# Performance work log

Hardware: AMD Instinct MI355X
Metric: run time of the kernel (lower is better)

## Reference

```python
import jax, jax.numpy as jnp
import numpy as np
from jax import lax


def log_g(x):
    # log of g(x) = x + 0.5 for x >= 0, sigmoid(x) for x < 0
    return jnp.where(x >= 0, jnp.log(jax.nn.relu(x) + 0.5), -jax.nn.softplus(-x))


def setup_inputs() -> dict:
    key = jax.random.key(0)
    k1, k2, k3, k4 = jax.random.split(key, 4)
    N, L, H_in, H = 8, 4096, 1024, 1024
    x = jax.random.normal(k1, (N, L, H_in), dtype=jnp.float32)
    W = jax.random.normal(k2, (2 * H, H_in), dtype=jnp.float32) * (1.0 / np.sqrt(H_in))
    b = jax.random.normal(k3, (2 * H,), dtype=jnp.float32) * 0.01
    hx = jax.random.uniform(k4, (N, H), dtype=jnp.float32)  # positive initial state
    return {"x": x, "W": W, "b": b, "hx": hx}


def reference(x, W, b, hx):
    # linear_ih: (N, L, 2H)
    zh = jnp.einsum('nli,oi->nlo', x, W) + b
    z, h_inter = jnp.split(zh, 2, axis=-1)  # each (N, L, H)
    log_z = -jax.nn.softplus(-z)            # log sigmoid(z)
    log_coeffs = -jax.nn.softplus(z)        # log (1 - sigmoid(z))
    log_h0 = jnp.log(hx)[:, None, :]        # (N, 1, H)
    log_tilde_h = log_g(h_inter)
    log_values = jnp.concatenate([log_h0, log_z + log_tilde_h], axis=1)  # (N, L+1, H)
    # Heinsen parallel scan in log space
    a_star = jnp.pad(jnp.cumsum(log_coeffs, axis=1), ((0, 0), (1, 0), (0, 0)))  # (N, L+1, H)
    log_h = a_star + lax.cumlogsumexp(log_values - a_star, axis=1)
    h = jnp.exp(log_h)
    return h[:, 1:]  # (N, L, H)
```

## Files before the change

### kernel.cpp

```cpp
#include <hip/hip_runtime.h>
#include <hip/hip_bf16.h>
#include <hip/hip_fp16.h>


#define N_B   8
#define L_SEQ 4096
#define H_DIM 1024
#define K_DIM 1024
#define O_DIM 2048
#define M_TOT (N_B * L_SEQ)

#define BM 128
#define BN 128
#define BK 64

#define NCHUNK 128
#define CLEN   (L_SEQ / NCHUNK)
#define NCH    (N_B * H_DIM)

typedef unsigned short ushort_t;
typedef unsigned short us8 __attribute__((ext_vector_type(8)));
typedef __bf16 v8bf __attribute__((ext_vector_type(8)));
typedef float f32x4 __attribute__((ext_vector_type(4)));

static __device__ __forceinline__ ushort_t f2bf(float f) {
    __hip_bfloat16 h = __float2bfloat16(f);
    return *reinterpret_cast<ushort_t*>(&h);
}

static __device__ __forceinline__ void dma16(const ushort_t* g, ushort_t* l) {
    __builtin_amdgcn_global_load_lds(
        (const __attribute__((address_space(1))) unsigned int*)g,
        (__attribute__((address_space(3))) unsigned int*)l,
        16, 0, 0);
}

__global__ __launch_bounds__(256) void cvt_f32_bf16(
    const float* __restrict__ src, ushort_t* __restrict__ dst)
{
    const int i = blockIdx.x * 256 + threadIdx.x;
    const float4 f0 = ((const float4*)src)[2 * i];
    const float4 f1 = ((const float4*)src)[2 * i + 1];
    us8 o;
    o[0] = f2bf(f0.x); o[1] = f2bf(f0.y); o[2] = f2bf(f0.z); o[3] = f2bf(f0.w);
    o[4] = f2bf(f1.x); o[5] = f2bf(f1.y); o[6] = f2bf(f1.z); o[7] = f2bf(f1.w);
    ((us8*)dst)[i] = o;
}

__global__ __launch_bounds__(256) void cvt_w_perm(
    const float* __restrict__ src, ushort_t* __restrict__ dst,
    const float* __restrict__ b, float* __restrict__ bp)
{
    const int i  = blockIdx.x * 256 + threadIdx.x;
    const int op = i >> 7;
    const int k  = (i & 127) * 8;
    const int B  = op >> 4, t = op & 15;
    const int orig = (B & 1) * 1024 + (B >> 1) * 16 + t;
    const float4* s = (const float4*)(src + (size_t)orig * K_DIM + k);
    const float4 f0 = s[0], f1 = s[1];
    us8 o;
    o[0] = f2bf(f0.x); o[1] = f2bf(f0.y); o[2] = f2bf(f0.z); o[3] = f2bf(f0.w);
    o[4] = f2bf(f1.x); o[5] = f2bf(f1.y); o[6] = f2bf(f1.z); o[7] = f2bf(f1.w);
    *(us8*)(dst + (size_t)op * K_DIM + k) = o;

    if (i < O_DIM) {
        const int Bb = i >> 4, tb = i & 15;
        bp[i] = b[(Bb & 1) * 1024 + (Bb >> 1) * 16 + tb];
    }
}

__device__ __forceinline__ void gate_av(float z, float hi, float& a, float& v)
{
    const float e  = __expf(-z);
    const float sz = 1.0f / (1.0f + e);
    a = e * sz;
    const float g = (hi >= 0.0f) ? (hi + 0.5f)
                                 : (1.0f / (1.0f + __expf(-hi)));
    v = sz * g;
}

__global__ __launch_bounds__(256) void gemm_zh(
    const ushort_t* __restrict__ Xb,
    const ushort_t* __restrict__ Wb,
    const float* __restrict__ biasp,
    __half2* __restrict__ avbuf,
    float* __restrict__ Aar,
    float* __restrict__ Bar,
    int mbase)
{
    __shared__ ushort_t As[BM * BK];
    __shared__ ushort_t Bs[BN * BK];

    const int tid    = threadIdx.x;
    const int wave   = tid >> 6;
    const int lane   = tid & 63;
    const int lane15 = lane & 15;
    const int quad   = lane >> 4;

    const int n0 = blockIdx.x * BN;
    const int m0 = (blockIdx.y + mbase) * BM;

    const int lrow = lane >> 3;
    const int jj   = (lane & 7) ^ lrow;
    const ushort_t* gA = Xb + (size_t)(m0 + wave * 8 + lrow) * K_DIM + jj * 8;
    const ushort_t* gB = Wb + (size_t)(n0 + wave * 8 + lrow) * K_DIM + jj * 8;
    ushort_t* lA = &As[(wave * 8) * BK];
    ushort_t* lB = &Bs[(wave * 8) * BK];

    const int wm = (wave >> 1) * 64;
    const int wn = (wave & 1) * 64;

    int offA[2][4], offB[2][4];
#pragma unroll
    for (int s = 0; s < 2; ++s) {
#pragma unroll
        for (int t = 0; t < 4; ++t) {
            const int rowA = wm + t * 16 + lane15;
            offA[s][t] = rowA * BK + (((s * 4 + quad) ^ (rowA & 7)) * 8);
            const int rowB = wn + t * 16 + lane15;
            offB[s][t] = rowB * BK + (((s * 4 + quad) ^ (rowB & 7)) * 8);
        }
    }

    const f32x4 fzero = {0.f, 0.f, 0.f, 0.f};
    f32x4 acc[4][4];
#pragma unroll
    for (int i = 0; i < 4; ++i)
#pragma unroll
        for (int j = 0; j < 4; ++j)
            acc[i][j] = fzero;

    for (int kt = 0; kt < K_DIM / BK; ++kt) {
        __syncthreads();
#pragma unroll
        for (int r = 0; r < 4; ++r) {
            dma16(gA + (size_t)r * 32 * K_DIM + kt * BK, lA + r * 32 * BK);
            dma16(gB + (size_t)r * 32 * K_DIM + kt * BK, lB + r * 32 * BK);
        }
        __syncthreads();

#pragma unroll
        for (int s = 0; s < 2; ++s) {
            v8bf af[4], bfr[4];
#pragma unroll
            for (int t = 0; t < 4; ++t) af[t]  = *(const v8bf*)(&As[offA[s][t]]);
#pragma unroll
            for (int t = 0; t < 4; ++t) bfr[t] = *(const v8bf*)(&Bs[offB[s][t]]);
#pragma unroll
            for (int i = 0; i < 4; ++i)
#pragma unroll
                for (int j = 0; j < 4; ++j)
                    acc[i][j] = __builtin_amdgcn_mfma_f32_16x16x32_bf16(
                        af[i], bfr[j], acc[i][j], 0, 0, 0);
        }
    }

    float bv[4];
#pragma unroll
    for (int j = 0; j < 4; ++j)
        bv[j] = biasp[n0 + wn + j * 16 + lane15];

    const int chbase = ((n0 + wn) >> 1) + lane15;

    float Ai[4][2], Bi[4][2];

#pragma unroll
    for (int i = 0; i < 4; ++i) {
        float A[2] = {1.f, 1.f};
        float Bc[2] = {0.f, 0.f};
#pragma unroll
        for (int r = 0; r < 4; ++r) {
            const size_t row = (size_t)(m0 + wm + i * 16 + quad * 4 + r);
            __half2* prow = avbuf + row * H_DIM + chbase;
#pragma unroll
            for (int jp = 0; jp < 2; ++jp) {
                const float z  = acc[i][2 * jp][r]     + bv[2 * jp];
                const float hh = acc[i][2 * jp + 1][r] + bv[2 * jp + 1];
                float a, v;
                gate_av(z, hh, a, v);
                const __half2 h2 = __floats2half2_rn(a, v);
                prow[jp * 16] = h2;
                const float2 f = __half22float2(h2);
                Bc[jp] = fmaf(f.x, Bc[jp], f.y);
                A[jp] *= f.x;
            }
        }
#pragma unroll
        for (int jp = 0; jp < 2; ++jp) {
#pragma unroll
            for (int d = 16; d < 64; d <<= 1) {
                const float Ay = __shfl_xor(A[jp],  d);
                const float By = __shfl_xor(Bc[jp], d);
                Bc[jp] = (lane & d) ? fmaf(A[jp], By, Bc[jp])
                                    : fmaf(Ay, Bc[jp], By);
                A[jp] *= Ay;
            }
            Ai[i][jp] = A[jp];
            Bi[i][jp] = Bc[jp];
        }
    }

    if (lane < 16) {
#pragma unroll
        for (int cc = 0; cc < 2; ++cc) {
            const int grow = m0 + wm + cc * 32;
            const int n    = grow >> 12;
            const int cch  = (grow & (L_SEQ - 1)) >> 5;
            const size_t o = (size_t)cch * NCH + (size_t)n * H_DIM + chbase;
#pragma unroll
            for (int jp = 0; jp < 2; ++jp) {
                const float A0 = Ai[2 * cc][jp],     B0 = Bi[2 * cc][jp];
                const float A1 = Ai[2 * cc + 1][jp], B1 = Bi[2 * cc + 1][jp];
                Aar[o + jp * 16] = A1 * A0;
                Bar[o + jp * 16] = fmaf(A1, B0, B1);
            }
        }
    }
}

__global__ __launch_bounds__(256) void scan_phase2(
    const float* __restrict__ Aar, const float* __restrict__ Bar,
    const float* __restrict__ hx, float* __restrict__ seed)
{
    const int ch = blockIdx.x * 256 + threadIdx.x;
    float carry = hx[ch];
#pragma unroll 8
    for (int c = 0; c < NCHUNK; ++c) {
        seed[c * NCH + ch] = carry;
        carry = fmaf(Aar[c * NCH + ch], carry, Bar[c * NCH + ch]);
    }
}

__global__ __launch_bounds__(256) void scan_phase3(
    const __half2* __restrict__ avbuf,
    const float* __restrict__ seed, float* __restrict__ out)
{
    const int idx = blockIdx.x * 256 + threadIdx.x;
    const int h4  = (idx & 255) << 2;
    const int n   = (idx >> 8) & 7;
    const int c   = idx >> 11;
    const size_t base = ((size_t)(n * L_SEQ + c * CLEN)) * H_DIM + h4;
    const float4* avp = (const float4*)(avbuf + base);
    float* op = out + base;

    const size_t so = (size_t)c * NCH + n * H_DIM + h4;
    float h0[4];
    *(f32x4*)h0 = *(const f32x4*)(seed + so);

#pragma unroll 8
    for (int s = 0; s < CLEN; ++s) {
        float4 avr = avp[(size_t)s * (H_DIM / 4)];
        const __half2* a2 = (const __half2*)&avr;
#pragma unroll
        for (int j = 0; j < 4; ++j) {
            const float2 av = __half22float2(a2[j]);
            h0[j] = fmaf(av.x, h0[j], av.y);
        }
        f32x4 hv = *(const f32x4*)h0;
        __builtin_nontemporal_store(hv, (f32x4*)(op + (size_t)s * H_DIM));
    }
}

extern "C" void kernel_launch(void* const* d_in, const int* in_sizes, int n_in,
                              void* d_out, int out_size, void* d_ws, size_t ws_size,
                              hipStream_t stream)
{
    const float* X    = (const float*)d_in[0];
    const float* Wm   = (const float*)d_in[1];
    const float* bias = (const float*)d_in[2];
    const float* hx   = (const float*)d_in[3];
    float* out = (float*)d_out;

    char* ws = (char*)d_ws;
    ushort_t* wb   = (ushort_t*)ws;
    __half2*  avbuf = (__half2*)(ws + (size_t)O_DIM * K_DIM * 2);
    float*    seed = (float*)((char*)avbuf + (size_t)M_TOT * H_DIM * 4);
    float*    biasp = seed + (size_t)NCHUNK * NCH;

    ushort_t* xb = (ushort_t*)d_out;
    float* Aar = out + (size_t)M_TOT * H_DIM / 2;
    float* Bar = Aar + (size_t)NCHUNK * NCH;

    cvt_w_perm<<<O_DIM * K_DIM / 8 / 256, 256, 0, stream>>>(Wm, wb, bias, biasp);
    cvt_f32_bf16<<<M_TOT * K_DIM / 8 / 256, 256, 0, stream>>>(X, xb);

    dim3 ggrid(O_DIM / BN, (M_TOT / BM) / 4);
    for (int q = 0; q < 4; ++q)
        gemm_zh<<<ggrid, 256, 0, stream>>>(xb, wb, biasp, avbuf, Aar, Bar,
                                           q * 64);

    scan_phase2<<<NCH / 256, 256, 0, stream>>>(Aar, Bar, hx, seed);

    const int p3_blocks = (NCH / 4) * NCHUNK / 256;
    scan_phase3<<<p3_blocks, 256, 0, stream>>>(avbuf, seed, out);
}
```

Before: 478.1 us.

## Double-buffer GEMM with 256-wide tiles, 8 waves, and interleaved DMA/MFMA schedule

```diff
diff --git a/kernel.cpp b/kernel.cpp
--- a/kernel.cpp
+++ b/kernel.cpp
@@ -11,8 +11,9 @@
 #define M_TOT (N_B * L_SEQ)
 
 #define BM 128
-#define BN 128
+#define BN 256
 #define BK 64
+#define KTILES (K_DIM / BK)
 
 #define NCHUNK 128
 #define CLEN   (L_SEQ / NCHUNK)
@@ -79,48 +80,100 @@
     v = sz * g;
 }
 
-__global__ __launch_bounds__(256) void gemm_zh(
+
+#define STG_A(b, kt, r) dma16(gA + (size_t)(r) * 64 * K_DIM + (size_t)(kt) * BK, \
+                              &As[b][((r) * 64 + wave * 8) * BK])
+#define STG_B(b, kt, r) dma16(gB + (size_t)(r) * 64 * K_DIM + (size_t)(kt) * BK, \
+                              &Bs[b][((r) * 64 + wave * 8) * BK])
+
+#define RD_HALF(NA, NB, rb, h)                                                \
+    _Pragma("unroll") for (int i2_ = 0; i2_ < 2; ++i2_)                       \
+    _Pragma("unroll") for (int s_ = 0; s_ < 2; ++s_) {                        \
+        NA[(h) * 2 + i2_][s_] = *(const v8bf*)&As[rb][offA[(h) * 2 + i2_][s_]]; \
+        NB[(h) * 2 + i2_][s_] = *(const v8bf*)&Bs[rb][offB[(h) * 2 + i2_][s_]]; \
+    }
+
+#define QUAD(p, CA, CB) {                                                     \
+    const int ih_ = (p) >> 1, jh_ = (p) & 1;                                  \
+    _Pragma("unroll") for (int i2_ = 0; i2_ < 2; ++i2_)                       \
+    _Pragma("unroll") for (int j2_ = 0; j2_ < 2; ++j2_)                       \
+    _Pragma("unroll") for (int s_ = 0; s_ < 2; ++s_)                          \
+        acc[ih_ * 2 + i2_][jh_ * 2 + j2_] =                                   \
+            __builtin_amdgcn_mfma_f32_16x16x32_bf16(                          \
+                CA[ih_ * 2 + i2_][s_], CB[jh_ * 2 + j2_][s_],                 \
+                acc[ih_ * 2 + i2_][jh_ * 2 + j2_], 0, 0, 0); }
+
+#define BAR() __builtin_amdgcn_s_barrier()
+#define PRIO(x) __builtin_amdgcn_s_setprio(x)
+
+#define TILE(t, cb, CA, CB, NA, NB, sg, rd)                                   \
+    {                                                                         \
+                                                                      \
+        if (sg) { STG_A(cb, (t) + 2, 0); STG_A(cb, (t) + 2, 1); }             \
+        BAR();                                                                \
+        PRIO(1); QUAD(0, CA, CB); PRIO(0);                                    \
+        BAR();                                                                \
+                                                                      \
+        if (sg) { STG_B(cb, (t) + 2, 0); STG_B(cb, (t) + 2, 1); }             \
+        BAR();                                                                \
+        PRIO(1); QUAD(1, CA, CB); PRIO(0);                                    \
+        BAR();                                                                \
+                                                                      \
+        if (sg) { STG_B(cb, (t) + 2, 2); }                                    \
+        if (rd) {                                                             \
+            if (sg) { asm volatile("s_waitcnt vmcnt(5)" ::: "memory"); }      \
+            else    { asm volatile("s_waitcnt vmcnt(0)" ::: "memory"); }      \
+            RD_HALF(NA, NB, (cb) ^ 1, 0);                                     \
+        }                                                                     \
+        BAR();                                                                \
+        PRIO(1); QUAD(2, CA, CB); PRIO(0);                                    \
+        BAR();                                                                \
+                                                                      \
+        if (sg) { STG_B(cb, (t) + 2, 3); }                                    \
+        if (rd) { RD_HALF(NA, NB, (cb) ^ 1, 1); }                             \
+        asm volatile("s_waitcnt lgkmcnt(0)" ::: "memory");                    \
+        __builtin_amdgcn_sched_barrier(0);                                    \
+        PRIO(1); QUAD(3, CA, CB); PRIO(0);                                    \
+        BAR();                                                                \
+    }
+
+__global__ __launch_bounds__(512, 2) void gemm_zh(
     const ushort_t* __restrict__ Xb,
     const ushort_t* __restrict__ Wb,
     const float* __restrict__ biasp,
     __half2* __restrict__ avbuf,
     float* __restrict__ Aar,
-    float* __restrict__ Bar,
-    int mbase)
-{
-    __shared__ ushort_t As[BM * BK];
-    __shared__ ushort_t Bs[BN * BK];
+    float* __restrict__ Bar)
+{
+    __shared__ ushort_t As[2][BM * BK];
+    __shared__ ushort_t Bs[2][BN * BK];
 
     const int tid    = threadIdx.x;
     const int wave   = tid >> 6;
     const int lane   = tid & 63;
     const int lane15 = lane & 15;
     const int quad   = lane >> 4;
+    const int wm     = (wave >> 2) * 64;
+    const int wn     = (wave & 3) * 64;
 
     const int n0 = blockIdx.x * BN;
-    const int m0 = (blockIdx.y + mbase) * BM;
+    const int m0 = blockIdx.y * BM;
 
     const int lrow = lane >> 3;
     const int jj   = (lane & 7) ^ lrow;
     const ushort_t* gA = Xb + (size_t)(m0 + wave * 8 + lrow) * K_DIM + jj * 8;
     const ushort_t* gB = Wb + (size_t)(n0 + wave * 8 + lrow) * K_DIM + jj * 8;
-    ushort_t* lA = &As[(wave * 8) * BK];
-    ushort_t* lB = &Bs[(wave * 8) * BK];
-
-    const int wm = (wave >> 1) * 64;
-    const int wn = (wave & 1) * 64;
-
-    int offA[2][4], offB[2][4];
-#pragma unroll
-    for (int s = 0; s < 2; ++s) {
-#pragma unroll
-        for (int t = 0; t < 4; ++t) {
-            const int rowA = wm + t * 16 + lane15;
-            offA[s][t] = rowA * BK + (((s * 4 + quad) ^ (rowA & 7)) * 8);
-            const int rowB = wn + t * 16 + lane15;
-            offB[s][t] = rowB * BK + (((s * 4 + quad) ^ (rowB & 7)) * 8);
-        }
-    }
+
+    int offA[4][2], offB[4][2];
+#pragma unroll
+    for (int i = 0; i < 4; ++i)
+#pragma unroll
+        for (int s = 0; s < 2; ++s) {
+            const int rA = wm + i * 16 + lane15;
+            offA[i][s] = rA * BK + (((s * 4 + quad) ^ (rA & 7)) * 8);
+            const int rB = wn + i * 16 + lane15;
+            offB[i][s] = rB * BK + (((s * 4 + quad) ^ (rB & 7)) * 8);
+        }
 
     const f32x4 fzero = {0.f, 0.f, 0.f, 0.f};
     f32x4 acc[4][4];
@@ -130,29 +183,29 @@
         for (int j = 0; j < 4; ++j)
             acc[i][j] = fzero;
 
-    for (int kt = 0; kt < K_DIM / BK; ++kt) {
-        __syncthreads();
-#pragma unroll
-        for (int r = 0; r < 4; ++r) {
-            dma16(gA + (size_t)r * 32 * K_DIM + kt * BK, lA + r * 32 * BK);
-            dma16(gB + (size_t)r * 32 * K_DIM + kt * BK, lB + r * 32 * BK);
-        }
-        __syncthreads();
-
-#pragma unroll
-        for (int s = 0; s < 2; ++s) {
-            v8bf af[4], bfr[4];
-#pragma unroll
-            for (int t = 0; t < 4; ++t) af[t]  = *(const v8bf*)(&As[offA[s][t]]);
-#pragma unroll
-            for (int t = 0; t < 4; ++t) bfr[t] = *(const v8bf*)(&Bs[offB[s][t]]);
-#pragma unroll
-            for (int i = 0; i < 4; ++i)
-#pragma unroll
-                for (int j = 0; j < 4; ++j)
-                    acc[i][j] = __builtin_amdgcn_mfma_f32_16x16x32_bf16(
-                        af[i], bfr[j], acc[i][j], 0, 0, 0);
-        }
+    v8bf a0[4][2], b0[4][2], a1[4][2], b1[4][2];
+
+#pragma unroll
+    for (int r = 0; r < 2; ++r) STG_A(0, 0, r);
+#pragma unroll
+    for (int r = 0; r < 4; ++r) STG_B(0, 0, r);
+#pragma unroll
+    for (int r = 0; r < 2; ++r) STG_A(1, 1, r);
+#pragma unroll
+    for (int r = 0; r < 4; ++r) STG_B(1, 1, r);
+    asm volatile("s_waitcnt vmcnt(6)" ::: "memory");
+    BAR();
+    RD_HALF(a0, b0, 0, 0);
+    RD_HALF(a0, b0, 0, 1);
+    asm volatile("s_waitcnt lgkmcnt(0)" ::: "memory");
+    BAR();
+
+#pragma unroll 1
+    for (int tt = 0; tt < KTILES / 2; ++tt) {
+        const int  t0 = 2 * tt, t1 = 2 * tt + 1;
+        const bool sg = (tt < KTILES / 2 - 1);
+        TILE(t0, 0, a0, b0, a1, b1, sg, true);
+        TILE(t1, 1, a1, b1, a0, b0, sg, sg);
     }
 
     float bv[4];
@@ -284,10 +337,8 @@
     cvt_w_perm<<<O_DIM * K_DIM / 8 / 256, 256, 0, stream>>>(Wm, wb, bias, biasp);
     cvt_f32_bf16<<<M_TOT * K_DIM / 8 / 256, 256, 0, stream>>>(X, xb);
 
-    dim3 ggrid(O_DIM / BN, (M_TOT / BM) / 4);
-    for (int q = 0; q < 4; ++q)
-        gemm_zh<<<ggrid, 256, 0, stream>>>(xb, wb, biasp, avbuf, Aar, Bar,
-                                           q * 64);
+    dim3 ggrid(O_DIM / BN, M_TOT / BM);
+    gemm_zh<<<ggrid, 512, 0, stream>>>(xb, wb, biasp, avbuf, Aar, Bar);
 
     scan_phase2<<<NCH / 256, 256, 0, stream>>>(Aar, Bar, hx, seed);
 
```

New measurement: 499.5 us. 1.04x slower.

## Rewrite GEMM as 256x256 tile with 512 threads and multi-buffered LDS pipeline

Applied to the files above, without the earlier changes.

```diff
diff --git a/kernel.cpp b/kernel.cpp
--- a/kernel.cpp
+++ b/kernel.cpp
@@ -10,9 +10,10 @@
 #define O_DIM 2048
 #define M_TOT (N_B * L_SEQ)
 
-#define BM 128
-#define BN 128
+#define BM 256
+#define BN 256
 #define BK 64
+#define KTILES (K_DIM / BK)
 
 #define NCHUNK 128
 #define CLEN   (L_SEQ / NCHUNK)
@@ -79,98 +80,133 @@
     v = sz * g;
 }
 
-__global__ __launch_bounds__(256) void gemm_zh(
+
+#define STG_A(P, tt, h) do {                                                  \
+    dma16(gA + (size_t)((h) * 128)      * K_DIM + (size_t)(tt) * BK,          \
+          &As[((P) * 2 + (h)) * 8192 + (wave * 8) * 64]);                     \
+    dma16(gA + (size_t)((h) * 128 + 64) * K_DIM + (size_t)(tt) * BK,          \
+          &As[((P) * 2 + (h)) * 8192 + (64 + wave * 8) * 64]);                \
+} while (0)
+#define STG_B(P, tt, h) do {                                                  \
+    dma16(gB + (size_t)((h) * 128)      * K_DIM + (size_t)(tt) * BK,          \
+          &Bs[((P) * 2 + (h)) * 8192 + (wave * 8) * 64]);                     \
+    dma16(gB + (size_t)((h) * 128 + 64) * K_DIM + (size_t)(tt) * BK,          \
+          &Bs[((P) * 2 + (h)) * 8192 + (64 + wave * 8) * 64]);                \
+} while (0)
+
+#define VM4 asm volatile("s_waitcnt vmcnt(4)" ::: "memory")
+#define VM0 asm volatile("s_waitcnt vmcnt(0)" ::: "memory")
+
+#define PHASE(P, iq, STGS, VMS)                                               \
+    {                                                                         \
+        v8bf af[2][2];                                                        \
+        if ((iq) == 0) {                                                      \
+            _Pragma("unroll") for (int j_ = 0; j_ < 4; ++j_)                  \
+            _Pragma("unroll") for (int s_ = 0; s_ < 2; ++s_)                  \
+                bfr[j_][s_] = *(const v8bf*)&Bs[bbase + (P) * 16384 +         \
+                                                j_ * 1024 + aoff[s_]];        \
+        }                                                                     \
+        _Pragma("unroll") for (int u_ = 0; u_ < 2; ++u_)                      \
+        _Pragma("unroll") for (int s_ = 0; s_ < 2; ++s_)                      \
+            af[u_][s_] = *(const v8bf*)&As[abase + (P) * 16384 +              \
+                                           ((iq) * 2 + u_) * 1024 + aoff[s_]];\
+        STGS;                                                                 \
+        VMS;                                                                  \
+        asm volatile("" ::: "memory");                                        \
+        __builtin_amdgcn_s_barrier();                                         \
+        asm volatile("s_waitcnt lgkmcnt(0)" ::: "memory");                    \
+        __builtin_amdgcn_sched_barrier(0);                                    \
+        __builtin_amdgcn_s_setprio(1);                                        \
+        _Pragma("unroll") for (int s_ = 0; s_ < 2; ++s_)                      \
+        _Pragma("unroll") for (int u_ = 0; u_ < 2; ++u_)                      \
+        _Pragma("unroll") for (int j_ = 0; j_ < 4; ++j_)                      \
+            acc[(iq) * 2 + u_][j_] = __builtin_amdgcn_mfma_f32_16x16x32_bf16( \
+                af[u_][s_], bfr[j_][s_], acc[(iq) * 2 + u_][j_], 0, 0, 0);    \
+        __builtin_amdgcn_s_setprio(0);                                        \
+        __builtin_amdgcn_s_barrier();                                         \
+    }
+
+#define TILE(t, P, SGA, SGB, VMS)                                             \
+    PHASE(P, 0, { if (SGA) STG_A((P) ^ 1, (t) + 1, 0); }, {});                \
+    PHASE(P, 1, { if (SGA) STG_A((P) ^ 1, (t) + 1, 1); }, {});                \
+    PHASE(P, 2, { if (SGB) STG_B((P), (t) + 2, 0); }, {});                    \
+    PHASE(P, 3, { if (SGB) STG_B((P), (t) + 2, 1); }, VMS);
+
+__global__ __launch_bounds__(512, 2) void gemm_zh(
     const ushort_t* __restrict__ Xb,
     const ushort_t* __restrict__ Wb,
     const float* __restrict__ biasp,
     __half2* __restrict__ avbuf,
     float* __restrict__ Aar,
-    float* __restrict__ Bar,
-    int mbase)
-{
-    __shared__ ushort_t As[BM * BK];
-    __shared__ ushort_t Bs[BN * BK];
+    float* __restrict__ Bar)
+{
+    __shared__ ushort_t As[4 * 8192];
+    __shared__ ushort_t Bs[4 * 8192];
 
     const int tid    = threadIdx.x;
     const int wave   = tid >> 6;
     const int lane   = tid & 63;
     const int lane15 = lane & 15;
     const int quad   = lane >> 4;
+    const int wr     = wave >> 2;
+    const int wc     = wave & 3;
 
     const int n0 = blockIdx.x * BN;
-    const int m0 = (blockIdx.y + mbase) * BM;
+    const int m0 = blockIdx.y * BM;
 
     const int lrow = lane >> 3;
     const int jj   = (lane & 7) ^ lrow;
     const ushort_t* gA = Xb + (size_t)(m0 + wave * 8 + lrow) * K_DIM + jj * 8;
     const ushort_t* gB = Wb + (size_t)(n0 + wave * 8 + lrow) * K_DIM + jj * 8;
-    ushort_t* lA = &As[(wave * 8) * BK];
-    ushort_t* lB = &Bs[(wave * 8) * BK];
-
-    const int wm = (wave >> 1) * 64;
-    const int wn = (wave & 1) * 64;
-
-    int offA[2][4], offB[2][4];
-#pragma unroll
-    for (int s = 0; s < 2; ++s) {
-#pragma unroll
-        for (int t = 0; t < 4; ++t) {
-            const int rowA = wm + t * 16 + lane15;
-            offA[s][t] = rowA * BK + (((s * 4 + quad) ^ (rowA & 7)) * 8);
-            const int rowB = wn + t * 16 + lane15;
-            offB[s][t] = rowB * BK + (((s * 4 + quad) ^ (rowB & 7)) * 8);
-        }
-    }
+
+    int aoff[2];
+#pragma unroll
+    for (int s = 0; s < 2; ++s)
+        aoff[s] = lane15 * 64 + (((s * 4 + quad) ^ (lane15 & 7)) * 8);
+    const int abase = wr * 8192;
+    const int bbase = (wc >> 1) * 8192 + (wc & 1) * 4096;
 
     const f32x4 fzero = {0.f, 0.f, 0.f, 0.f};
-    f32x4 acc[4][4];
-#pragma unroll
-    for (int i = 0; i < 4; ++i)
+    f32x4 acc[8][4];
+#pragma unroll
+    for (int i = 0; i < 8; ++i)
 #pragma unroll
         for (int j = 0; j < 4; ++j)
             acc[i][j] = fzero;
 
-    for (int kt = 0; kt < K_DIM / BK; ++kt) {
-        __syncthreads();
-#pragma unroll
-        for (int r = 0; r < 4; ++r) {
-            dma16(gA + (size_t)r * 32 * K_DIM + kt * BK, lA + r * 32 * BK);
-            dma16(gB + (size_t)r * 32 * K_DIM + kt * BK, lB + r * 32 * BK);
-        }
-        __syncthreads();
-
-#pragma unroll
-        for (int s = 0; s < 2; ++s) {
-            v8bf af[4], bfr[4];
-#pragma unroll
-            for (int t = 0; t < 4; ++t) af[t]  = *(const v8bf*)(&As[offA[s][t]]);
-#pragma unroll
-            for (int t = 0; t < 4; ++t) bfr[t] = *(const v8bf*)(&Bs[offB[s][t]]);
-#pragma unroll
-            for (int i = 0; i < 4; ++i)
-#pragma unroll
-                for (int j = 0; j < 4; ++j)
-                    acc[i][j] = __builtin_amdgcn_mfma_f32_16x16x32_bf16(
-                        af[i], bfr[j], acc[i][j], 0, 0, 0);
-        }
-    }
+    v8bf bfr[4][2];
+
+    STG_A(0, 0, 0); STG_A(0, 0, 1);
+    STG_B(0, 0, 0); STG_B(0, 0, 1);
+    STG_B(1, 1, 0); STG_B(1, 1, 1);
+    VM4;
+    __builtin_amdgcn_s_barrier();
+
+#pragma unroll 1
+    for (int tt = 0; tt < 7; ++tt) {
+        const int t0 = 2 * tt;
+        TILE(t0,     0, 1, 1, VM4);
+        TILE(t0 + 1, 1, 1, 1, VM4);
+    }
+    TILE(14, 0, 1, 0, VM0);
+    TILE(15, 1, 0, 0, {});
 
     float bv[4];
 #pragma unroll
     for (int j = 0; j < 4; ++j)
-        bv[j] = biasp[n0 + wn + j * 16 + lane15];
-
-    const int chbase = ((n0 + wn) >> 1) + lane15;
-
-    float Ai[4][2], Bi[4][2];
-
-#pragma unroll
-    for (int i = 0; i < 4; ++i) {
+        bv[j] = biasp[n0 + wc * 64 + j * 16 + lane15];
+
+    const int chbase = ((n0 + wc * 64) >> 1) + lane15;
+
+    float Ai[8][2], Bi[8][2];
+
+#pragma unroll
+    for (int i = 0; i < 8; ++i) {
         float A[2] = {1.f, 1.f};
         float Bc[2] = {0.f, 0.f};
 #pragma unroll
         for (int r = 0; r < 4; ++r) {
-            const size_t row = (size_t)(m0 + wm + i * 16 + quad * 4 + r);
+            const size_t row = (size_t)(m0 + wr * 128 + i * 16 + quad * 4 + r);
             __half2* prow = avbuf + row * H_DIM + chbase;
 #pragma unroll
             for (int jp = 0; jp < 2; ++jp) {
@@ -202,8 +238,8 @@
 
     if (lane < 16) {
 #pragma unroll
-        for (int cc = 0; cc < 2; ++cc) {
-            const int grow = m0 + wm + cc * 32;
+        for (int cc = 0; cc < 4; ++cc) {
+            const int grow = m0 + wr * 128 + cc * 32;
             const int n    = grow >> 12;
             const int cch  = (grow & (L_SEQ - 1)) >> 5;
             const size_t o = (size_t)cch * NCH + (size_t)n * H_DIM + chbase;
@@ -284,10 +320,8 @@
     cvt_w_perm<<<O_DIM * K_DIM / 8 / 256, 256, 0, stream>>>(Wm, wb, bias, biasp);
     cvt_f32_bf16<<<M_TOT * K_DIM / 8 / 256, 256, 0, stream>>>(X, xb);
 
-    dim3 ggrid(O_DIM / BN, (M_TOT / BM) / 4);
-    for (int q = 0; q < 4; ++q)
-        gemm_zh<<<ggrid, 256, 0, stream>>>(xb, wb, biasp, avbuf, Aar, Bar,
-                                           q * 64);
+    dim3 ggrid(O_DIM / BN, M_TOT / BM);
+    gemm_zh<<<ggrid, 512, 0, stream>>>(xb, wb, biasp, avbuf, Aar, Bar);
 
     scan_phase2<<<NCH / 256, 256, 0, stream>>>(Aar, Bar, hx, seed);
 
```

New measurement: 440.1 us. 8.0% less time.
